# Performance work log

Measured on AMD Instinct MI355X. Metric: run time of the kernel, lower is better.

## Reference

```python
import jax, jax.numpy as jnp
import numpy as np

C0, C1 = 8, 4            # scalar / vector channels (type_in = type_out = [8,4])
K = 5                    # p-space kernel size
G = 8                    # number of gaussian radial basis functions
EPS = 1e-6               # zero-length epsilon
R_MAX = 5.5              # max |p_off - q_diff| ~ sqrt(3)*2 + 2


def _levi_civita():
    e = np.zeros((3, 3, 3), np.float32)
    e[0, 1, 2] = e[1, 2, 0] = e[2, 0, 1] = 1.0
    e[0, 2, 1] = e[2, 1, 0] = e[1, 0, 2] = -1.0
    return jnp.asarray(e)


def setup_inputs() -> dict:
    key = jax.random.key(0)
    ks = jax.random.split(key, 10)
    N, Q, P = 1, 16, 8
    dim = C0 + 3 * C1
    x = jax.random.normal(ks[0], (N, dim, Q, P, P, P), jnp.float32)

    def qschema(k):
        q = jax.random.normal(k, (Q, 3), jnp.float32)
        return q / jnp.max(jnp.linalg.norm(q, axis=-1))  # normalize lengths to <= 1

    q_in, q_out = qschema(ks[1]), qschema(ks[2])
    s = 0.1
    w_ss = s * jax.random.normal(ks[3], (C0, C0, G), jnp.float32)
    w_vs = s * jax.random.normal(ks[4], (C1, C0, G), jnp.float32)
    w_sv = s * jax.random.normal(ks[5], (C0, C1, G), jnp.float32)
    w_vv0 = s * jax.random.normal(ks[6], (C1, C1, G), jnp.float32)
    w_vv1 = s * jax.random.normal(ks[7], (C1, C1, G), jnp.float32)
    bias = s * jax.random.normal(ks[8], (C0,), jnp.float32)
    return dict(x=x, q_in=q_in, q_out=q_out, w_ss=w_ss, w_vs=w_vs, w_sv=w_sv,
                w_vv0=w_vv0, w_vv1=w_vv1, bias=bias)


def reference(x, q_in, q_out, w_ss, w_vs, w_sv, w_vv0, w_vv1, bias):
    N, dim_in, Qi = x.shape[0], x.shape[1], x.shape[2]
    Qo = q_out.shape[0]
    K3 = K ** 3
    # p-space tap offsets (voxel units, zyx) of the 5x5x5 kernel
    offs = jnp.arange(K, dtype=x.dtype) - (K - 1) / 2.0
    oz, oy, ox = jnp.meshgrid(offs, offs, offs, indexing='ij')
    p_off = jnp.stack([oz, oy, ox], -1).reshape(-1, 3)                       # (K3,3)
    # pq_diff geometry: v = p_offset - (q_out - q_in)
    v = p_off[None, None] - (q_out[:, None, None] - q_in[None, :, None])     # (Qo,Qi,K3,3)
    r = jnp.linalg.norm(v, axis=-1)                                          # (Qo,Qi,K3)
    u = jnp.where(r[..., None] > EPS, v / jnp.maximum(r, EPS)[..., None], 0.0)
    # gaussian radial basis on |v|
    centers = jnp.linspace(0.0, R_MAX, G).astype(x.dtype)
    sigma = R_MAX / (G - 1)
    R = jnp.exp(-0.5 * ((r[..., None] - centers) / sigma) ** 2)              # (Qo,Qi,K3,G)
    RY = R[..., None] * u[..., None, :]                                      # (Qo,Qi,K3,G,3) radial x Y_1
    eye3 = jnp.eye(3, dtype=x.dtype)
    eps3 = _levi_civita().astype(x.dtype)
    # CG paths (l_in,l_out,l_f): axes a=out ch, c=in ch, p=Qo, q=Qi, k=tap, g=radial, m/n/i/j=vec comps
    K_ss = jnp.einsum('acg,pqkg->apcqk', w_ss, R)                            # (0,0,0)
    K_vs = jnp.einsum('acg,pqkgm->ampcqk', w_vs, RY)                         # (0,1,1)
    K_sv = jnp.einsum('acg,pqkgm->apcmqk', w_sv, RY)                         # (1,0,1)
    K_vv = (jnp.einsum('acg,pqkg,mn->ampcnqk', w_vv0, R, eye3)               # (1,1,0) identity
            + 0.7071067811865476 *
            jnp.einsum('acg,pqkgm,imj->aipcjqk', w_vv1, RY, eps3))           # (1,1,1) cross prod
    top = jnp.concatenate([K_ss, K_sv.reshape(C0, Qo, 3 * C1, Qi, K3)], axis=2)
    bot = jnp.concatenate([K_vs.reshape(3 * C1, Qo, C0, Qi, K3),
                           K_vv.reshape(3 * C1, Qo, 3 * C1, Qi, K3)], axis=2)
    kern = jnp.concatenate([top, bot], axis=0)                               # (dim_out,Qo,dim_in,Qi,K3)
    dim_out = C0 + 3 * C1
    kern = kern.reshape(dim_out * Qo, dim_in * Qi, K, K, K)
    xr = x.reshape(N, dim_in * Qi, *x.shape[3:])
    out = jax.lax.conv_general_dilated(
        xr, kern, window_strides=(1, 1, 1), padding='SAME',
        dimension_numbers=('NCDHW', 'OIDHW', 'NCDHW'))
    out = out.reshape(N, dim_out, Qo, *x.shape[3:])
    b_full = jnp.concatenate([bias, jnp.zeros(3 * C1, bias.dtype)])
    return out + b_full.reshape(1, dim_out, 1, 1, 1, 1)
```

## Files before the change

kernel.cpp:

```cpp
#include <hip/hip_runtime.h>
#include <hip/hip_bf16.h>
#include <math.h>

#define C0 8
#define C1 4
#define NCH 20
#define NQ 16
#define K3 125
#define G 8
#define RMAX 5.5f
#define EPSL 1e-6f

#define KD1 2048
#define PHI_N 1048576
#define XTP_N 552960
#define W2_N 20480
#define OUT_N 163840
#define E2C_B 10485760

#define LDS_A 18432
#define LDS_B 27648

using f32x4 = __attribute__((ext_vector_type(4))) float;
using s16x8 = __attribute__((ext_vector_type(8))) short;

__device__ __forceinline__ float epsf(int i, int m, int j) {
    if (i == m || m == j || i == j) return 0.f;
    return (m == (i + 1) % 3) ? 1.f : -1.f;
}

__global__ __launch_bounds__(256) void prep_kernel(
    const float* __restrict__ x,
    const float* __restrict__ q_in, const float* __restrict__ q_out,
    const float* __restrict__ w_ss, const float* __restrict__ w_vs,
    const float* __restrict__ w_sv, const float* __restrict__ w_vv0,
    const float* __restrict__ w_vv1, const float* __restrict__ bias,
    __hip_bfloat16* __restrict__ phi, __hip_bfloat16* __restrict__ xtp,
    __hip_bfloat16* __restrict__ w2, float* __restrict__ out)
{
    int gid = blockIdx.x * 256 + threadIdx.x;
    if (gid < PHI_N) {
        int col = gid & (KD1 - 1); int m = gid >> 11;
        int t = col >> 4, q = col & 15;
        int p = m >> 5,  b = m & 31;
        int g = b >> 2,  mi = b & 3;
        float val = 0.f;
        if (t < K3) {
            int tz = t / 25, ty = (t / 5) % 5, tx = t % 5;
            float vz = (float)(tz - 2) - (q_out[p*3+0] - q_in[q*3+0]);
            float vy = (float)(ty - 2) - (q_out[p*3+1] - q_in[q*3+1]);
            float vx = (float)(tx - 2) - (q_out[p*3+2] - q_in[q*3+2]);
            float r  = sqrtf(vz*vz + vy*vy + vx*vx);
            float inv = (r > EPSL) ? (1.0f / r) : 0.0f;
            const float sigma = RMAX / (float)(G - 1);
            float d = (r - (RMAX * (float)g / (float)(G - 1))) / sigma;
            float Rg = expf(-0.5f * d * d);
            float u = (mi == 1) ? vz*inv : ((mi == 2) ? vy*inv : vx*inv);
            val = (mi == 0) ? Rg : Rg * u;
        }
        phi[gid] = __float2bfloat16(val);
    } else if (gid < PHI_N + XTP_N) {
        int g2 = gid - PHI_N;
        int q = g2 & 15; int r = g2 >> 4;
        int ax = r % 12; r /= 12;
        int ay = r % 12; r /= 12;
        int az = r % 12; int c = r / 12;
        int iz = az - 2, iy = ay - 2, ix = ax - 2;
        bool valid = ((unsigned)iz < 8u) & ((unsigned)iy < 8u) & ((unsigned)ix < 8u);
        float v = valid ? x[((c * NQ + q) << 9) + (iz << 6) + (iy << 3) + ix] : 0.f;
        xtp[g2] = __float2bfloat16(v);
    } else if (gid < PHI_N + XTP_N + W2_N) {
        int id = gid - (PHI_N + XTP_N);
        int b = id & 31; int r = id >> 5;
        int c = r % NCH; int o = r / NCH;
        int g = b >> 2,  mi = b & 3;
        float val = 0.f;
        if (o < NCH) {
            if (o < C0) {
                if (c < C0) { if (mi == 0) val = w_ss[(o * C0 + c) * G + g]; }
                else { int cv = (c - C0) / 3, j = (c - C0) % 3;
                       if (mi == 1 + j) val = w_sv[(o * C1 + cv) * G + g]; }
            } else {
                int ov = (o - C0) / 3, i = (o - C0) % 3;
                if (c < C0) { if (mi == 1 + i) val = w_vs[(ov * C0 + c) * G + g]; }
                else {
                    int cv = (c - C0) / 3, j = (c - C0) % 3;
                    if (mi == 0) { if (i == j) val = w_vv0[(ov * C1 + cv) * G + g]; }
                    else val = 0.7071067811865476f * w_vv1[(ov * C1 + cv) * G + g]
                               * epsf(i, mi - 1, j);
                }
            }
        }
        w2[id] = __float2bfloat16(val);
    } else {
        int id = gid - (PHI_N + XTP_N + W2_N);
        int o = id >> 13;
        out[id] = (o < C0) ? bias[o] : 0.f;
    }
}

__global__ __launch_bounds__(256, 3) void gemm1_kernel(
    const char* __restrict__ phi_b, const char* __restrict__ xtp_b,
    char* __restrict__ E2_b)
{
    __shared__ __align__(16) char lds[LDS_A + LDS_B];

    int tid = threadIdx.x;
    int wave = tid >> 6, lane = tid & 63;
    int row = lane & 15, quad = lane >> 4;
    int wi = wave >> 1, wj = wave & 1;

    int bi = blockIdx.x;
    int kc = bi / 320;
    int r  = bi - kc * 320;
    int pg = r / 80;
    int r2 = r - pg * 80;
    int c  = r2 >> 2;
    int zq = r2 & 3;

    {
        const char* src = xtp_b + c * 55296 + zq * 9216;
        for (int i = tid; i < 1728; i += 256)
            *(s16x8*)(lds + LDS_A + i * 16) = *(const s16x8*)(src + i * 16);
    }

    const char* abase = phi_b + (size_t)(pg * 128) * 4096 + kc * 2048;
    int srow[4], skp[4];
    #pragma unroll
    for (int i = 0; i < 4; ++i) { int s = tid + i * 256; srow[i] = s >> 3; skp[i] = s & 7; }
    s16x8 areg[4];
    #pragma unroll
    for (int i = 0; i < 4; ++i)
        areg[i] = *(const s16x8*)(abase + srow[i] * 4096 + skp[i] * 16);

    int bpre[4];
    #pragma unroll
    for (int nt = 0; nt < 4; ++nt) {
        int zl = wj * 64 + nt * 16 + row;
        int zz = zl >> 6, zy = (zl >> 3) & 7, zx = zl & 7;
        bpre[nt] = LDS_A + (zz * 144 + zy * 12 + zx) * 32 + (quad & 1) * 16;
    }
    int hi = quad >> 1;

    f32x4 acc[4][4];
    #pragma unroll
    for (int i = 0; i < 4; ++i)
        #pragma unroll
        for (int j = 0; j < 4; ++j) acc[i][j] = (f32x4){0.f, 0.f, 0.f, 0.f};

    for (int j = 0; j < 16; ++j) {
        int toff[4];
        #pragma unroll
        for (int tt = 0; tt < 4; ++tt) {
            int t = kc * 64 + j * 4 + tt; if (t > 124) t = 124;
            int tz = t / 25, trm = t - tz * 25;
            int ty = trm / 5, tx = trm - ty * 5;
            toff[tt] = (tz * 144 + ty * 12 + tx) * 32;
        }
        #pragma unroll
        for (int i = 0; i < 4; ++i)
            *(s16x8*)(lds + srow[i] * 144 + skp[i] * 16) = areg[i];
        __syncthreads();
        if (j < 15) {
            #pragma unroll
            for (int i = 0; i < 4; ++i)
                areg[i] = *(const s16x8*)(abase + srow[i] * 4096 + (j + 1) * 128 + skp[i] * 16);
        }
        #pragma unroll
        for (int st = 0; st < 2; ++st) {
            s16x8 af[4], bf[4];
            #pragma unroll
            for (int mt = 0; mt < 4; ++mt)
                af[mt] = *(const s16x8*)(lds + (wi * 64 + mt * 16 + row) * 144
                                             + (st * 4 + quad) * 16);
            int tsel = toff[st * 2 + hi];
            #pragma unroll
            for (int nt = 0; nt < 4; ++nt)
                bf[nt] = *(const s16x8*)(lds + bpre[nt] + tsel);
            #pragma unroll
            for (int mt = 0; mt < 4; ++mt)
                #pragma unroll
                for (int nt = 0; nt < 4; ++nt)
                    acc[mt][nt] = __builtin_amdgcn_mfma_f32_16x16x32_bf16(
                        af[mt], bf[nt], acc[mt][nt], 0, 0, 0);
        }
        __syncthreads();
    }

    int wbase = wave * 8704;
    #pragma unroll
    for (int mt = 0; mt < 4; ++mt) {
        #pragma unroll
        for (int nt = 0; nt < 4; ++nt) {
            int zl = nt * 16 + row;
            union { unsigned long long u; __hip_bfloat16 h[4]; } pk;
            pk.h[0] = __float2bfloat16(acc[mt][nt][0]);
            pk.h[1] = __float2bfloat16(acc[mt][nt][1]);
            pk.h[2] = __float2bfloat16(acc[mt][nt][2]);
            pk.h[3] = __float2bfloat16(acc[mt][nt][3]);
            *(unsigned long long*)(lds + wbase + zl * 136 + (mt * 16 + quad * 4) * 2) = pk.u;
        }
    }
    char* Ek = E2_b + (size_t)kc * E2C_B;
    int pbase = pg * 4 + wi * 2;
    #pragma unroll
    for (int it = 0; it < 8; ++it) {
        int item = lane + it * 64;
        int piece = item & 3;
        int zl = (item >> 2) & 63;
        int h  = item >> 8;
        s16x8 v = *(const s16x8*)(lds + wbase + zl * 136 + h * 64 + piece * 16);
        int p = pbase + h;
        int z = zq * 128 + wj * 64 + zl;
        *(s16x8*)(Ek + ((size_t)((p * NCH + c) << 9) + z) * 64 + piece * 16) = v;
    }
}

__global__ __launch_bounds__(128) void gemm2_kernel(
    const char* __restrict__ w2_b, const char* __restrict__ E2_b,
    float* __restrict__ out)
{
    int tid = threadIdx.x;
    int wave = tid >> 6, lane = tid & 63;
    int row = lane & 15, quad = lane >> 4;
    int bi = blockIdx.x;
    int p  = bi >> 6;
    int zb = (bi >> 2) & 15;
    int kc = (bi >> 1) & 1;
    int ch = bi & 1;
    int z  = zb * 32 + wave * 16 + row;

    const char* bbase = E2_b + (size_t)kc * E2C_B + (size_t)p * 655360
                        + (size_t)z * 64 + quad * 16;

    f32x4 acc[2];
    acc[0] = (f32x4){0.f, 0.f, 0.f, 0.f};
    acc[1] = (f32x4){0.f, 0.f, 0.f, 0.f};

    #pragma unroll 5
    for (int ci = 0; ci < 10; ++ci) {
        int cc = ch * 10 + ci;
        s16x8 a0 = *(const s16x8*)(w2_b + (row)      * 1280 + cc * 64 + quad * 16);
        s16x8 a1 = *(const s16x8*)(w2_b + (16 + row) * 1280 + cc * 64 + quad * 16);
        s16x8 b  = *(const s16x8*)(bbase + (size_t)cc * 32768);
        acc[0] = __builtin_amdgcn_mfma_f32_16x16x32_bf16(a0, b, acc[0], 0, 0, 0);
        acc[1] = __builtin_amdgcn_mfma_f32_16x16x32_bf16(a1, b, acc[1], 0, 0, 0);
    }

    #pragma unroll
    for (int mt = 0; mt < 2; ++mt)
        #pragma unroll
        for (int ri = 0; ri < 4; ++ri) {
            int o = mt * 16 + quad * 4 + ri;
            if (o < NCH)
                atomicAdd(out + ((o * NQ + p) << 9) + z, acc[mt][ri]);
        }
}

extern "C" void kernel_launch(void* const* d_in, const int* in_sizes, int n_in,
                              void* d_out, int out_size, void* d_ws, size_t ws_size,
                              hipStream_t stream) {
    const float* x     = (const float*)d_in[0];
    const float* q_in  = (const float*)d_in[1];
    const float* q_out = (const float*)d_in[2];
    const float* w_ss  = (const float*)d_in[3];
    const float* w_vs  = (const float*)d_in[4];
    const float* w_sv  = (const float*)d_in[5];
    const float* w_vv0 = (const float*)d_in[6];
    const float* w_vv1 = (const float*)d_in[7];
    const float* bias  = (const float*)d_in[8];
    float* out = (float*)d_out;

    char* ws = (char*)d_ws;
    __hip_bfloat16* phi = (__hip_bfloat16*)(ws + 0);
    __hip_bfloat16* xtp = (__hip_bfloat16*)(ws + 2097152);
    __hip_bfloat16* w2  = (__hip_bfloat16*)(ws + 3203072);
    char*           E2  = (char*)(ws + 3244032);

    const int PREP_N = PHI_N + XTP_N + W2_N + OUT_N;
    hipLaunchKernelGGL(prep_kernel, dim3(PREP_N / 256), dim3(256), 0, stream,
                       x, q_in, q_out, w_ss, w_vs, w_sv, w_vv0, w_vv1, bias,
                       phi, xtp, w2, out);
    hipLaunchKernelGGL(gemm1_kernel, dim3(640), dim3(256), 0, stream,
                       (const char*)phi, (const char*)xtp, E2);
    hipLaunchKernelGGL(gemm2_kernel, dim3(1024), dim3(128), 0, stream,
                       (const char*)w2, (const char*)E2, out);
}
```

Measured before the change: 115.5 us.

## Load GEMM1 A fragments directly from global, swizzle LDS, drop gemm2 atomics

GEMM1 no longer stages the phi operand through LDS. Each wave loads its MFMA A fragments straight from global memory into registers, double-buffered across k-steps, which removes the per-iteration LDS store and both barriers. The xtp tile in LDS now uses an XOR swizzle to reduce bank conflicts, and LDS size drops while launch bounds go from 3 to 2 blocks per SM. GEMM2 now reduces over both k-chunks and all channels inside one block and writes the output with bias folded in, which removes the atomics and the output-init pass in prep. The trade-off is fewer, longer gemm2 blocks (256 instead of 1024) and more register pressure in gemm1.

```diff
diff --git a/kernel.cpp b/kernel.cpp
--- a/kernel.cpp
+++ b/kernel.cpp
@@ -15,11 +15,9 @@
 #define PHI_N 1048576
 #define XTP_N 552960
 #define W2_N 20480
-#define OUT_N 163840
 #define E2C_B 10485760
 
-#define LDS_A 18432
-#define LDS_B 27648
+#define LDS_SZ 34816
 
 using f32x4 = __attribute__((ext_vector_type(4))) float;
 using s16x8 = __attribute__((ext_vector_type(8))) short;
@@ -34,9 +32,9 @@
     const float* __restrict__ q_in, const float* __restrict__ q_out,
     const float* __restrict__ w_ss, const float* __restrict__ w_vs,
     const float* __restrict__ w_sv, const float* __restrict__ w_vv0,
-    const float* __restrict__ w_vv1, const float* __restrict__ bias,
+    const float* __restrict__ w_vv1,
     __hip_bfloat16* __restrict__ phi, __hip_bfloat16* __restrict__ xtp,
-    __hip_bfloat16* __restrict__ w2, float* __restrict__ out)
+    __hip_bfloat16* __restrict__ w2)
 {
     int gid = blockIdx.x * 256 + threadIdx.x;
     if (gid < PHI_N) {
@@ -69,7 +67,7 @@
         bool valid = ((unsigned)iz < 8u) & ((unsigned)iy < 8u) & ((unsigned)ix < 8u);
         float v = valid ? x[((c * NQ + q) << 9) + (iz << 6) + (iy << 3) + ix] : 0.f;
         xtp[g2] = __float2bfloat16(v);
-    } else if (gid < PHI_N + XTP_N + W2_N) {
+    } else {
         int id = gid - (PHI_N + XTP_N);
         int b = id & 31; int r = id >> 5;
         int c = r % NCH; int o = r / NCH;
@@ -92,23 +90,20 @@
             }
         }
         w2[id] = __float2bfloat16(val);
-    } else {
-        int id = gid - (PHI_N + XTP_N + W2_N);
-        int o = id >> 13;
-        out[id] = (o < C0) ? bias[o] : 0.f;
-    }
-}
-
-__global__ __launch_bounds__(256, 3) void gemm1_kernel(
+    }
+}
+
+__global__ __launch_bounds__(256, 2) void gemm1_kernel(
     const char* __restrict__ phi_b, const char* __restrict__ xtp_b,
     char* __restrict__ E2_b)
 {
-    __shared__ __align__(16) char lds[LDS_A + LDS_B];
+    __shared__ __align__(16) char lds[LDS_SZ];
 
     int tid = threadIdx.x;
     int wave = tid >> 6, lane = tid & 63;
     int row = lane & 15, quad = lane >> 4;
     int wi = wave >> 1, wj = wave & 1;
+    int hi = quad >> 1;
 
     int bi = blockIdx.x;
     int kc = bi / 320;
@@ -120,27 +115,22 @@
 
     {
         const char* src = xtp_b + c * 55296 + zq * 9216;
-        for (int i = tid; i < 1728; i += 256)
-            *(s16x8*)(lds + LDS_A + i * 16) = *(const s16x8*)(src + i * 16);
-    }
-
-    const char* abase = phi_b + (size_t)(pg * 128) * 4096 + kc * 2048;
-    int srow[4], skp[4];
-    #pragma unroll
-    for (int i = 0; i < 4; ++i) { int s = tid + i * 256; srow[i] = s >> 3; skp[i] = s & 7; }
-    s16x8 areg[4];
-    #pragma unroll
-    for (int i = 0; i < 4; ++i)
-        areg[i] = *(const s16x8*)(abase + srow[i] * 4096 + skp[i] * 16);
+        for (int i = tid; i < 1728; i += 256) {
+            int d = (i * 16) ^ (((i >> 1) & 7) << 4);
+            *(s16x8*)(lds + d) = *(const s16x8*)(src + i * 16);
+        }
+    }
+
+    const char* abase = phi_b + (size_t)(pg * 128 + wi * 64 + row) * 4096
+                        + kc * 2048 + quad * 16;
 
     int bpre[4];
     #pragma unroll
     for (int nt = 0; nt < 4; ++nt) {
         int zl = wj * 64 + nt * 16 + row;
         int zz = zl >> 6, zy = (zl >> 3) & 7, zx = zl & 7;
-        bpre[nt] = LDS_A + (zz * 144 + zy * 12 + zx) * 32 + (quad & 1) * 16;
-    }
-    int hi = quad >> 1;
+        bpre[nt] = (zz * 144 + zy * 12 + zx) * 32 + (quad & 1) * 16;
+    }
 
     f32x4 acc[4][4];
     #pragma unroll
@@ -148,44 +138,58 @@
         #pragma unroll
         for (int j = 0; j < 4; ++j) acc[i][j] = (f32x4){0.f, 0.f, 0.f, 0.f};
 
-    for (int j = 0; j < 16; ++j) {
-        int toff[4];
-        #pragma unroll
-        for (int tt = 0; tt < 4; ++tt) {
-            int t = kc * 64 + j * 4 + tt; if (t > 124) t = 124;
-            int tz = t / 25, trm = t - tz * 25;
-            int ty = trm / 5, tx = trm - ty * 5;
-            toff[tt] = (tz * 144 + ty * 12 + tx) * 32;
-        }
-        #pragma unroll
-        for (int i = 0; i < 4; ++i)
-            *(s16x8*)(lds + srow[i] * 144 + skp[i] * 16) = areg[i];
-        __syncthreads();
-        if (j < 15) {
-            #pragma unroll
-            for (int i = 0; i < 4; ++i)
-                areg[i] = *(const s16x8*)(abase + srow[i] * 4096 + (j + 1) * 128 + skp[i] * 16);
-        }
-        #pragma unroll
-        for (int st = 0; st < 2; ++st) {
-            s16x8 af[4], bf[4];
-            #pragma unroll
-            for (int mt = 0; mt < 4; ++mt)
-                af[mt] = *(const s16x8*)(lds + (wi * 64 + mt * 16 + row) * 144
-                                             + (st * 4 + quad) * 16);
-            int tsel = toff[st * 2 + hi];
-            #pragma unroll
-            for (int nt = 0; nt < 4; ++nt)
-                bf[nt] = *(const s16x8*)(lds + bpre[nt] + tsel);
-            #pragma unroll
-            for (int mt = 0; mt < 4; ++mt)
-                #pragma unroll
-                for (int nt = 0; nt < 4; ++nt)
-                    acc[mt][nt] = __builtin_amdgcn_mfma_f32_16x16x32_bf16(
-                        af[mt], bf[nt], acc[mt][nt], 0, 0, 0);
-        }
-        __syncthreads();
-    }
+    __syncthreads();
+
+    #define LOADA(Adst, jj) do {                                              \
+        _Pragma("unroll")                                                     \
+        for (int st_ = 0; st_ < 2; ++st_)                                     \
+            _Pragma("unroll")                                                 \
+            for (int mt_ = 0; mt_ < 4; ++mt_)                                 \
+                Adst[st_ * 4 + mt_] = *(const s16x8*)(abase + mt_ * 65536     \
+                                          + (jj) * 128 + st_ * 64);           \
+    } while (0)
+
+    #define COMPUTE(Asrc, jj) do {                                            \
+        int toff_[4];                                                         \
+        _Pragma("unroll")                                                     \
+        for (int tt_ = 0; tt_ < 4; ++tt_) {                                   \
+            int t_ = kc * 64 + (jj) * 4 + tt_; if (t_ > 124) t_ = 124;        \
+            int tz_ = t_ / 25, trm_ = t_ - tz_ * 25;                          \
+            int ty_ = trm_ / 5, tx_ = trm_ - ty_ * 5;                         \
+            toff_[tt_] = (tz_ * 144 + ty_ * 12 + tx_) * 32;                   \
+        }                                                                     \
+        _Pragma("unroll")                                                     \
+        for (int st_ = 0; st_ < 2; ++st_) {                                   \
+            s16x8 bf_[4];                                                     \
+            int tsel_ = toff_[st_ * 2 + hi];                                  \
+            _Pragma("unroll")                                                 \
+            for (int nt_ = 0; nt_ < 4; ++nt_) {                               \
+                int ba_ = bpre[nt_] + tsel_;                                  \
+                ba_ ^= ((ba_ >> 5) & 7) << 4;                                 \
+                bf_[nt_] = *(const s16x8*)(lds + ba_);                        \
+            }                                                                 \
+            _Pragma("unroll")                                                 \
+            for (int mt_ = 0; mt_ < 4; ++mt_)                                 \
+                _Pragma("unroll")                                             \
+                for (int nt_ = 0; nt_ < 4; ++nt_)                             \
+                    acc[mt_][nt_] = __builtin_amdgcn_mfma_f32_16x16x32_bf16(  \
+                        Asrc[st_ * 4 + mt_], bf_[nt_], acc[mt_][nt_], 0, 0, 0);\
+        }                                                                     \
+    } while (0)
+
+    s16x8 A0[8], A1[8];
+    LOADA(A0, 0);
+    for (int j = 0; j < 16; j += 2) {
+        LOADA(A1, j + 1);
+        COMPUTE(A0, j);
+        if (j + 2 < 16) LOADA(A0, j + 2);
+        COMPUTE(A1, j + 1);
+    }
+
+    #undef LOADA
+    #undef COMPUTE
+
+    __syncthreads();
 
     int wbase = wave * 8704;
     #pragma unroll
@@ -218,33 +222,32 @@
 
 __global__ __launch_bounds__(128) void gemm2_kernel(
     const char* __restrict__ w2_b, const char* __restrict__ E2_b,
-    float* __restrict__ out)
+    const float* __restrict__ bias, float* __restrict__ out)
 {
     int tid = threadIdx.x;
     int wave = tid >> 6, lane = tid & 63;
     int row = lane & 15, quad = lane >> 4;
     int bi = blockIdx.x;
-    int p  = bi >> 6;
-    int zb = (bi >> 2) & 15;
-    int kc = (bi >> 1) & 1;
-    int ch = bi & 1;
+    int p  = bi >> 4;
+    int zb = bi & 15;
     int z  = zb * 32 + wave * 16 + row;
 
-    const char* bbase = E2_b + (size_t)kc * E2C_B + (size_t)p * 655360
-                        + (size_t)z * 64 + quad * 16;
+    const char* bbase = E2_b + (size_t)p * 655360 + (size_t)z * 64 + quad * 16;
 
     f32x4 acc[2];
     acc[0] = (f32x4){0.f, 0.f, 0.f, 0.f};
     acc[1] = (f32x4){0.f, 0.f, 0.f, 0.f};
 
-    #pragma unroll 5
-    for (int ci = 0; ci < 10; ++ci) {
-        int cc = ch * 10 + ci;
-        s16x8 a0 = *(const s16x8*)(w2_b + (row)      * 1280 + cc * 64 + quad * 16);
-        s16x8 a1 = *(const s16x8*)(w2_b + (16 + row) * 1280 + cc * 64 + quad * 16);
-        s16x8 b  = *(const s16x8*)(bbase + (size_t)cc * 32768);
-        acc[0] = __builtin_amdgcn_mfma_f32_16x16x32_bf16(a0, b, acc[0], 0, 0, 0);
-        acc[1] = __builtin_amdgcn_mfma_f32_16x16x32_bf16(a1, b, acc[1], 0, 0, 0);
+    #pragma unroll
+    for (int kc = 0; kc < 2; ++kc) {
+        #pragma unroll 5
+        for (int cc = 0; cc < 20; ++cc) {
+            s16x8 a0 = *(const s16x8*)(w2_b + (row)      * 1280 + cc * 64 + quad * 16);
+            s16x8 a1 = *(const s16x8*)(w2_b + (16 + row) * 1280 + cc * 64 + quad * 16);
+            s16x8 b  = *(const s16x8*)(bbase + (size_t)kc * E2C_B + (size_t)cc * 32768);
+            acc[0] = __builtin_amdgcn_mfma_f32_16x16x32_bf16(a0, b, acc[0], 0, 0, 0);
+            acc[1] = __builtin_amdgcn_mfma_f32_16x16x32_bf16(a1, b, acc[1], 0, 0, 0);
+        }
     }
 
     #pragma unroll
@@ -252,8 +255,11 @@
         #pragma unroll
         for (int ri = 0; ri < 4; ++ri) {
             int o = mt * 16 + quad * 4 + ri;
-            if (o < NCH)
-                atomicAdd(out + ((o * NQ + p) << 9) + z, acc[mt][ri]);
+            if (o < NCH) {
+                float v = acc[mt][ri];
+                if (o < C0) v += bias[o];
+                out[((o * NQ + p) << 9) + z] = v;
+            }
         }
 }
 
@@ -277,12 +283,12 @@
     __hip_bfloat16* w2  = (__hip_bfloat16*)(ws + 3203072);
     char*           E2  = (char*)(ws + 3244032);
 
-    const int PREP_N = PHI_N + XTP_N + W2_N + OUT_N;
+    const int PREP_N = PHI_N + XTP_N + W2_N;
     hipLaunchKernelGGL(prep_kernel, dim3(PREP_N / 256), dim3(256), 0, stream,
-                       x, q_in, q_out, w_ss, w_vs, w_sv, w_vv0, w_vv1, bias,
-                       phi, xtp, w2, out);
+                       x, q_in, q_out, w_ss, w_vs, w_sv, w_vv0, w_vv1,
+                       phi, xtp, w2);
     hipLaunchKernelGGL(gemm1_kernel, dim3(640), dim3(256), 0, stream,
                        (const char*)phi, (const char*)xtp, E2);
-    hipLaunchKernelGGL(gemm2_kernel, dim3(1024), dim3(128), 0, stream,
-                       (const char*)w2, (const char*)E2, out);
-}
+    hipLaunchKernelGGL(gemm2_kernel, dim3(256), dim3(128), 0, stream,
+                       (const char*)w2, (const char*)E2, bias, out);
+}
```

Result: slower. 141.2 us (+22.2%).

## Swizzle LDS B tile and make gemm2 own full K with direct bias store

Applied to the files above, without the earlier changes.

The gemm1 B-operand LDS layout is XOR-swizzled on store and load to reduce bank conflicts on the fragment reads. gemm2 now loops over both K chunks and all 20 channels in a single block, so it writes the output directly with the bias added instead of zero-initialising out in prep and using atomicAdd. This removes the output init pass and the atomics, but gemm2 drops from 1024 to 256 blocks, each with a longer serial K loop, which lowers parallelism.

```diff
diff --git a/kernel.cpp b/kernel.cpp
--- a/kernel.cpp
+++ b/kernel.cpp
@@ -15,7 +15,6 @@
 #define PHI_N 1048576
 #define XTP_N 552960
 #define W2_N 20480
-#define OUT_N 163840
 #define E2C_B 10485760
 
 #define LDS_A 18432
@@ -34,9 +33,9 @@
     const float* __restrict__ q_in, const float* __restrict__ q_out,
     const float* __restrict__ w_ss, const float* __restrict__ w_vs,
     const float* __restrict__ w_sv, const float* __restrict__ w_vv0,
-    const float* __restrict__ w_vv1, const float* __restrict__ bias,
+    const float* __restrict__ w_vv1,
     __hip_bfloat16* __restrict__ phi, __hip_bfloat16* __restrict__ xtp,
-    __hip_bfloat16* __restrict__ w2, float* __restrict__ out)
+    __hip_bfloat16* __restrict__ w2)
 {
     int gid = blockIdx.x * 256 + threadIdx.x;
     if (gid < PHI_N) {
@@ -69,7 +68,7 @@
         bool valid = ((unsigned)iz < 8u) & ((unsigned)iy < 8u) & ((unsigned)ix < 8u);
         float v = valid ? x[((c * NQ + q) << 9) + (iz << 6) + (iy << 3) + ix] : 0.f;
         xtp[g2] = __float2bfloat16(v);
-    } else if (gid < PHI_N + XTP_N + W2_N) {
+    } else {
         int id = gid - (PHI_N + XTP_N);
         int b = id & 31; int r = id >> 5;
         int c = r % NCH; int o = r / NCH;
@@ -92,10 +91,6 @@
             }
         }
         w2[id] = __float2bfloat16(val);
-    } else {
-        int id = gid - (PHI_N + XTP_N + W2_N);
-        int o = id >> 13;
-        out[id] = (o < C0) ? bias[o] : 0.f;
     }
 }
 
@@ -120,8 +115,10 @@
 
     {
         const char* src = xtp_b + c * 55296 + zq * 9216;
-        for (int i = tid; i < 1728; i += 256)
-            *(s16x8*)(lds + LDS_A + i * 16) = *(const s16x8*)(src + i * 16);
+        for (int i = tid; i < 1728; i += 256) {
+            int d = (i * 16) ^ (((i >> 1) & 7) << 4);
+            *(s16x8*)(lds + LDS_A + d) = *(const s16x8*)(src + i * 16);
+        }
     }
 
     const char* abase = phi_b + (size_t)(pg * 128) * 4096 + kc * 2048;
@@ -175,8 +172,11 @@
                                              + (st * 4 + quad) * 16);
             int tsel = toff[st * 2 + hi];
             #pragma unroll
-            for (int nt = 0; nt < 4; ++nt)
-                bf[nt] = *(const s16x8*)(lds + bpre[nt] + tsel);
+            for (int nt = 0; nt < 4; ++nt) {
+                int ba = bpre[nt] + tsel;
+                ba ^= ((ba >> 5) & 7) << 4;
+                bf[nt] = *(const s16x8*)(lds + ba);
+            }
             #pragma unroll
             for (int mt = 0; mt < 4; ++mt)
                 #pragma unroll
@@ -218,33 +218,32 @@
 
 __global__ __launch_bounds__(128) void gemm2_kernel(
     const char* __restrict__ w2_b, const char* __restrict__ E2_b,
-    float* __restrict__ out)
+    const float* __restrict__ bias, float* __restrict__ out)
 {
     int tid = threadIdx.x;
     int wave = tid >> 6, lane = tid & 63;
     int row = lane & 15, quad = lane >> 4;
     int bi = blockIdx.x;
-    int p  = bi >> 6;
-    int zb = (bi >> 2) & 15;
-    int kc = (bi >> 1) & 1;
-    int ch = bi & 1;
+    int p  = bi >> 4;
+    int zb = bi & 15;
     int z  = zb * 32 + wave * 16 + row;
 
-    const char* bbase = E2_b + (size_t)kc * E2C_B + (size_t)p * 655360
-                        + (size_t)z * 64 + quad * 16;
+    const char* bbase = E2_b + (size_t)p * 655360 + (size_t)z * 64 + quad * 16;
 
     f32x4 acc[2];
     acc[0] = (f32x4){0.f, 0.f, 0.f, 0.f};
     acc[1] = (f32x4){0.f, 0.f, 0.f, 0.f};
 
-    #pragma unroll 5
-    for (int ci = 0; ci < 10; ++ci) {
-        int cc = ch * 10 + ci;
-        s16x8 a0 = *(const s16x8*)(w2_b + (row)      * 1280 + cc * 64 + quad * 16);
-        s16x8 a1 = *(const s16x8*)(w2_b + (16 + row) * 1280 + cc * 64 + quad * 16);
-        s16x8 b  = *(const s16x8*)(bbase + (size_t)cc * 32768);
-        acc[0] = __builtin_amdgcn_mfma_f32_16x16x32_bf16(a0, b, acc[0], 0, 0, 0);
-        acc[1] = __builtin_amdgcn_mfma_f32_16x16x32_bf16(a1, b, acc[1], 0, 0, 0);
+    #pragma unroll
+    for (int kc = 0; kc < 2; ++kc) {
+        #pragma unroll 5
+        for (int cc = 0; cc < 20; ++cc) {
+            s16x8 a0 = *(const s16x8*)(w2_b + (row)      * 1280 + cc * 64 + quad * 16);
+            s16x8 a1 = *(const s16x8*)(w2_b + (16 + row) * 1280 + cc * 64 + quad * 16);
+            s16x8 b  = *(const s16x8*)(bbase + (size_t)kc * E2C_B + (size_t)cc * 32768);
+            acc[0] = __builtin_amdgcn_mfma_f32_16x16x32_bf16(a0, b, acc[0], 0, 0, 0);
+            acc[1] = __builtin_amdgcn_mfma_f32_16x16x32_bf16(a1, b, acc[1], 0, 0, 0);
+        }
     }
 
     #pragma unroll
@@ -252,8 +251,11 @@
         #pragma unroll
         for (int ri = 0; ri < 4; ++ri) {
             int o = mt * 16 + quad * 4 + ri;
-            if (o < NCH)
-                atomicAdd(out + ((o * NQ + p) << 9) + z, acc[mt][ri]);
+            if (o < NCH) {
+                float v = acc[mt][ri];
+                if (o < C0) v += bias[o];
+                out[((o * NQ + p) << 9) + z] = v;
+            }
         }
 }
 
@@ -277,12 +279,12 @@
     __hip_bfloat16* w2  = (__hip_bfloat16*)(ws + 3203072);
     char*           E2  = (char*)(ws + 3244032);
 
-    const int PREP_N = PHI_N + XTP_N + W2_N + OUT_N;
+    const int PREP_N = PHI_N + XTP_N + W2_N;
     hipLaunchKernelGGL(prep_kernel, dim3(PREP_N / 256), dim3(256), 0, stream,
-                       x, q_in, q_out, w_ss, w_vs, w_sv, w_vv0, w_vv1, bias,
-                       phi, xtp, w2, out);
+                       x, q_in, q_out, w_ss, w_vs, w_sv, w_vv0, w_vv1,
+                       phi, xtp, w2);
     hipLaunchKernelGGL(gemm1_kernel, dim3(640), dim3(256), 0, stream,
                        (const char*)phi, (const char*)xtp, E2);
-    hipLaunchKernelGGL(gemm2_kernel, dim3(1024), dim3(128), 0, stream,
-                       (const char*)w2, (const char*)E2, out);
-}
+    hipLaunchKernelGGL(gemm2_kernel, dim3(256), dim3(128), 0, stream,
+                       (const char*)w2, (const char*)E2, bias, out);
+}
```

Measured after the change: 117.3 us. No clear change (+1.5%).
